# Performance work log

Hardware: AMD Instinct MI355X
Metric: run time of the kernel (lower is better)

Reference implementation:

```python
import jax, jax.numpy as jnp
import numpy as np

B, S = 2, 1024
V, H = 32000, 1024
NH, NKV = 16, 8
HD = H // NH          # 64
L = 8
I = 4 * H             # 4096
EPS = 1e-6
THETA = 10000.0
NEG = -1e9


def setup_inputs() -> dict:
    key = jax.random.key(0)
    ks = jax.random.split(key, 12)
    std = 0.02
    f = lambda k, shape: jax.random.normal(k, shape, jnp.float32) * std
    return {
        "input_ids": jax.random.randint(ks[0], (B, S), 0, V, dtype=jnp.int32),
        "embed": f(ks[1], (V, H)),
        "Wq": f(ks[2], (L, H, NH * HD)),
        "Wk": f(ks[3], (L, H, NKV * HD)),
        "Wv": f(ks[4], (L, H, NKV * HD)),
        "Wo": f(ks[5], (L, NH * HD, H)),
        "Wg": f(ks[6], (L, H, I)),
        "Wu": f(ks[7], (L, H, I)),
        "Wd": f(ks[8], (L, I, H)),
        "ln1": jnp.ones((L, H), jnp.float32),
        "ln2": jnp.ones((L, H), jnp.float32),
        "norm_w": jnp.ones((H,), jnp.float32),
        "lm_head": f(ks[9], (H, V)),
    }


def _rmsnorm(x, w):
    var = jnp.mean(x * x, axis=-1, keepdims=True)
    return x * jax.lax.rsqrt(var + EPS) * w


def _rotate_half(x):
    x1, x2 = jnp.split(x, 2, axis=-1)
    return jnp.concatenate((-x2, x1), axis=-1)


def reference(input_ids, embed, Wq, Wk, Wv, Wo, Wg, Wu, Wd, ln1, ln2, norm_w, lm_head):
    # RoPE tables [S, HD] (freqs duplicated, matching cat((freqs, freqs)))
    inv_freq = 1.0 / (THETA ** (jnp.arange(0, HD, 2, dtype=jnp.float32) / HD))
    t = jnp.arange(S, dtype=jnp.float32)
    freqs = t[:, None] * inv_freq[None, :]
    emb = jnp.concatenate((freqs, freqs), axis=-1)
    cos = jnp.cos(emb)[None, None]  # [1,1,S,HD]
    sin = jnp.sin(emb)[None, None]
    # causal mask [S, S]
    mask = jnp.where(jnp.tril(jnp.ones((S, S), bool)), 0.0, NEG).astype(jnp.float32)

    def layer(h, p):
        wq, wk, wv, wo, wg, wu, wd, g1, g2 = p
        x = _rmsnorm(h, g1)
        q = (x @ wq).reshape(B, S, NH, HD).transpose(0, 2, 1, 3)   # [B,NH,S,HD]
        k = (x @ wk).reshape(B, S, NKV, HD).transpose(0, 2, 1, 3)  # [B,NKV,S,HD]
        v = (x @ wv).reshape(B, S, NKV, HD).transpose(0, 2, 1, 3)
        q = q * cos + _rotate_half(q) * sin
        k = k * cos + _rotate_half(k) * sin
        rep = NH // NKV
        k = jnp.repeat(k, rep, axis=1)  # GQA repeat_interleave
        v = jnp.repeat(v, rep, axis=1)
        scores = jnp.einsum("bhqd,bhkd->bhqk", q, k) / np.sqrt(HD) + mask
        probs = jax.nn.softmax(scores, axis=-1)
        o = jnp.einsum("bhqk,bhkd->bhqd", probs, v)
        o = o.transpose(0, 2, 1, 3).reshape(B, S, NH * HD)
        h = h + o @ wo
        x = _rmsnorm(h, g2)
        h = h + (jax.nn.silu(x @ wg) * (x @ wu)) @ wd
        return h, None

    h = embed[input_ids]  # [B,S,H]
    h, _ = jax.lax.scan(layer, h, (Wq, Wk, Wv, Wo, Wg, Wu, Wd, ln1, ln2))
    h = _rmsnorm(h, norm_w)
    return h @ lm_head  # logits [B,S,V]
```

## Files before the change

### kernel.cpp

```cpp
#include <hip/hip_runtime.h>


typedef unsigned short u16;
typedef __bf16  bf16x8 __attribute__((ext_vector_type(8)));
typedef unsigned short u16x8 __attribute__((ext_vector_type(8)));
typedef float   f32x4  __attribute__((ext_vector_type(4)));

#define DEV static __device__ __forceinline__

constexpr int NB  = 2;
constexpr int S   = 1024;
constexpr int NT  = NB * S;
constexpr int H   = 1024;
constexpr int NH  = 16;
constexpr int NKV = 8;
constexpr int HD  = 64;
constexpr int NL  = 8;
constexpr int FF  = 4096;
constexpr int V   = 32000;
constexpr int QKVW = 2048;

DEV float b2f(u16 x) { return __uint_as_float(((unsigned)x) << 16); }
DEV u16   f2b(float f) {
  unsigned i = __float_as_uint(f);
  return (u16)((i + 0x7fffu + ((i >> 16) & 1u)) >> 16);
}

DEV void gload16(const void* g, void* l) {
  __builtin_amdgcn_global_load_lds(
      (const __attribute__((address_space(1))) void*)g,
      (__attribute__((address_space(3))) void*)l, 16, 0, 0);
}

DEV bf16x8 ld128(const u16* p) { return *reinterpret_cast<const bf16x8*>(p); }

template <int EPI>
__global__ __launch_bounds__(512, 2) void gemm256_k(
    const u16* __restrict__ A, int lda,
    const u16* __restrict__ Bt, int ldb,
    void* __restrict__ C, int ldc, int K)
{
  __shared__ __align__(16) u16 Asm[4][256 * 32];
  __shared__ __align__(16) u16 Bsm[4][256 * 32];

  const int tid  = threadIdx.x;
  const int lane = tid & 63;
  const int lrow = lane & 15;
  const int g    = lane >> 4;
  const int wid  = tid >> 6;
  const int wm   = wid >> 2, wn = wid & 3;

  int flat = blockIdx.y * gridDim.x + blockIdx.x;
  const int cpx = (gridDim.x * gridDim.y) >> 3;
  flat = (flat & 7) * cpx + (flat >> 3);
  const int bx = flat % gridDim.x;
  const int by = flat / gridDim.x;

  const int r0   = tid >> 2, pp = tid & 3;
  const int row1 = 128 + (tid >> 2);
  const int p0 = pp ^ ((r0 ^ (r0 >> 2)) & 3);
  const int p1 = pp ^ ((row1 ^ (row1 >> 2)) & 3);
  const u16* aS0 = A  + (size_t)(bx * 256 + r0)   * lda + p0 * 8;
  const u16* aS1 = A  + (size_t)(bx * 256 + row1) * lda + p1 * 8;
  const u16* bS0 = Bt + (size_t)(by * 256 + r0)   * ldb + p0 * 8;
  const u16* bS1 = Bt + (size_t)(by * 256 + row1) * ldb + p1 * 8;
  const int aB0 = tid * 16, aB1 = (512 + tid) * 16;

  int aOff[8], bOff[4];
  #pragma unroll
  for (int fm = 0; fm < 8; fm++) {
    const int r = wm * 128 + fm * 16 + lrow;
    aOff[fm] = r * 32 + (g ^ ((r ^ (r >> 2)) & 3)) * 8;
  }
  #pragma unroll
  for (int fn = 0; fn < 4; fn++) {
    const int r = wn * 64 + fn * 16 + lrow;
    bOff[fn] = r * 32 + (g ^ ((r ^ (r >> 2)) & 3)) * 8;
  }

  f32x4 acc[8][4] = {};
  const int ntk = K / 32;

  #pragma unroll
  for (int ts = 0; ts < 3; ts++) {
    const long kt = (long)ts * 32;
    gload16(aS0 + kt, (char*)Asm[ts] + aB0);
    gload16(bS0 + kt, (char*)Bsm[ts] + aB0);
    gload16(aS1 + kt, (char*)Asm[ts] + aB1);
    gload16(bS1 + kt, (char*)Bsm[ts] + aB1);
  }
  asm volatile("s_waitcnt vmcnt(8)" ::: "memory");
  __builtin_amdgcn_s_barrier();

#define KTILE(VMW, STG)                                                         \
  {                                                                             \
    const int rs = t & 3, ss = (t + 3) & 3;                                     \
    const long kt = (long)(t + 3) * 32;                                         \
    bf16x8 af[4], bf[4];                                                        \
    _Pragma("unroll") for (int i = 0; i < 4; i++) bf[i] = ld128(&Bsm[rs][bOff[i]]); \
    _Pragma("unroll") for (int i = 0; i < 4; i++) af[i] = ld128(&Asm[rs][aOff[i]]); \
    if (STG) { gload16(aS0 + kt, (char*)Asm[ss] + aB0);                         \
               gload16(bS0 + kt, (char*)Bsm[ss] + aB0); }                       \
    __builtin_amdgcn_s_barrier();                                               \
    asm volatile("s_waitcnt lgkmcnt(0)" ::: "memory");                          \
    __builtin_amdgcn_sched_barrier(0);                                          \
    __builtin_amdgcn_s_setprio(1);                                              \
    _Pragma("unroll") for (int m = 0; m < 4; m++)                               \
      _Pragma("unroll") for (int n = 0; n < 4; n++)                             \
        acc[m][n] = __builtin_amdgcn_mfma_f32_16x16x32_bf16(af[m], bf[n], acc[m][n], 0, 0, 0); \
    __builtin_amdgcn_s_setprio(0);                                              \
    __builtin_amdgcn_s_barrier();                                               \
    _Pragma("unroll") for (int i = 0; i < 4; i++) af[i] = ld128(&Asm[rs][aOff[4 + i]]); \
    if (STG) { gload16(aS1 + kt, (char*)Asm[ss] + aB1);                         \
               gload16(bS1 + kt, (char*)Bsm[ss] + aB1); }                       \
    __builtin_amdgcn_s_barrier();                                               \
    asm volatile("s_waitcnt lgkmcnt(0)" ::: "memory");                          \
    __builtin_amdgcn_sched_barrier(0);                                          \
    __builtin_amdgcn_s_setprio(1);                                              \
    _Pragma("unroll") for (int m = 0; m < 4; m++)                               \
      _Pragma("unroll") for (int n = 0; n < 4; n++)                             \
        acc[4 + m][n] = __builtin_amdgcn_mfma_f32_16x16x32_bf16(af[m], bf[n], acc[4 + m][n], 0, 0, 0); \
    __builtin_amdgcn_s_setprio(0);                                              \
    VMW;                                                                        \
    __builtin_amdgcn_sched_barrier(0);                                          \
    __builtin_amdgcn_s_barrier();                                               \
  }

  {
    int t = 0;
    for (; t < ntk - 3; ++t) KTILE(asm volatile("s_waitcnt vmcnt(8)" ::: "memory"), true);
    KTILE(asm volatile("s_waitcnt vmcnt(4)" ::: "memory"), false); ++t;
    KTILE(asm volatile("s_waitcnt vmcnt(0)" ::: "memory"), false); ++t;
    KTILE((void)0, false);
  }
#undef KTILE

  if (EPI == 2) {
    #pragma unroll
    for (int fm = 0; fm < 8; fm++) {
      #pragma unroll
      for (int fp = 0; fp < 2; fp++) {
        #pragma unroll
        for (int r = 0; r < 4; r++) {
          const size_t row = bx * 256 + wm * 128 + fm * 16 + g * 4 + r;
          const int nb = by * 256 + wn * 64 + fp * 32;
          const int oc = (nb >> 5) * 16 + lrow;
          const float gg = acc[fm][2 * fp][r];
          const float uu = acc[fm][2 * fp + 1][r];
          ((u16*)C)[row * ldc + oc] = f2b(gg / (1.f + __expf(-gg)) * uu);
        }
      }
    }
  } else {
    #pragma unroll
    for (int fm = 0; fm < 8; fm++) {
      #pragma unroll
      for (int fn = 0; fn < 4; fn++) {
        #pragma unroll
        for (int r = 0; r < 4; r++) {
          const size_t row = bx * 256 + wm * 128 + fm * 16 + g * 4 + r;
          const size_t col = by * 256 + wn * 64 + fn * 16 + lrow;
          ((float*)C)[row * ldc + col] = acc[fm][fn][r];
        }
      }
    }
  }
}

template <int BM, int BN, int WM, int WN, int EPI>
__global__ __launch_bounds__(256) void gemm_k(
    const u16* __restrict__ A, int lda,
    const u16* __restrict__ Bt, int ldb,
    void* __restrict__ C, int ldc,
    const float2* __restrict__ tab, int K)
{
  __shared__ __align__(16) u16 As[BM * 32];
  __shared__ __align__(16) u16 Bs[BN * 32];

  const int tid  = threadIdx.x;
  const int lane = tid & 63;
  const int lrow = lane & 15;
  const int kb   = lane >> 4;
  const int w    = tid >> 6;
  const int wm   = w / WN, wn = w % WN;
  constexpr int WR = BM / WM, WC = BN / WN;
  constexpr int FM = WR / 16, FN = WC / 16;

  const u16* Ap = A + blockIdx.x * BM * lda;
  const u16* Bp = Bt + blockIdx.y * BN * ldb;

  f32x4 acc[FM][FN] = {};

  for (int k0 = 0; k0 < K; k0 += 32) {
    #pragma unroll
    for (int i = 0; i < (BM * 4) / 256; i++) {
      const int c = i * 256 + tid;
      gload16(Ap + (c >> 2) * lda + k0 + (c & 3) * 8, (char*)As + c * 16);
    }
    #pragma unroll
    for (int i = 0; i < (BN * 4) / 256; i++) {
      const int c = i * 256 + tid;
      gload16(Bp + (c >> 2) * ldb + k0 + (c & 3) * 8, (char*)Bs + c * 16);
    }
    __syncthreads();

    bf16x8 af[FM], bfv[FN];
    #pragma unroll
    for (int fm = 0; fm < FM; fm++)
      af[fm] = *reinterpret_cast<const bf16x8*>(As + (wm * WR + fm * 16 + lrow) * 32 + kb * 8);
    #pragma unroll
    for (int fn = 0; fn < FN; fn++)
      bfv[fn] = *reinterpret_cast<const bf16x8*>(Bs + (wn * WC + fn * 16 + lrow) * 32 + kb * 8);

    #pragma unroll
    for (int fm = 0; fm < FM; fm++) {
      #pragma unroll
      for (int fn = 0; fn < FN; fn++) {
        acc[fm][fn] = __builtin_amdgcn_mfma_f32_16x16x32_bf16(af[fm], bfv[fn], acc[fm][fn], 0, 0, 0);
      }
    }
    __syncthreads();
  }

  if (EPI == 4) {
    const int colb = blockIdx.y * BN + wn * WC;
    const int head = colb >> 6;
    const float qs = (head < 16) ? 0.125f : 1.0f;
    #pragma unroll
    for (int fm = 0; fm < FM; fm++) {
      #pragma unroll
      for (int r = 0; r < 4; r++) {
        const int row = blockIdx.x * BM + wm * WR + fm * 16 + kb * 4 + r;
        if (head >= 24) {
          #pragma unroll
          for (int fn = 0; fn < FN; fn++)
            ((u16*)C)[row * ldc + colb + fn * 16 + lrow] = f2b(acc[fm][fn][r]);
        } else {
          const int s = row & (S - 1);
          #pragma unroll
          for (int fp = 0; fp < 2; fp++) {
            const int d = fp * 16 + lrow;
            const float2 cs = tab[s * 32 + d];
            const float x1 = acc[fm][fp][r];
            const float x2 = acc[fm][fp + 2][r];
            ((u16*)C)[row * ldc + colb + d]      = f2b((x1 * cs.x - x2 * cs.y) * qs);
            ((u16*)C)[row * ldc + colb + d + 32] = f2b((x2 * cs.x + x1 * cs.y) * qs);
          }
        }
      }
    }
  } else {
    #pragma unroll
    for (int fm = 0; fm < FM; fm++) {
      #pragma unroll
      for (int fn = 0; fn < FN; fn++) {
        #pragma unroll
        for (int r = 0; r < 4; r++) {
          const int row = blockIdx.x * BM + wm * WR + fm * 16 + kb * 4 + r;
          const int col = blockIdx.y * BN + wn * WC + fn * 16 + lrow;
          ((u16*)C)[row * ldc + col] = f2b(acc[fm][fn][r]);
        }
      }
    }
  }
}

__global__ __launch_bounds__(256) void transpose_k(
    const float* __restrict__ W, u16* __restrict__ WT, int K, int N, int rmode,
    size_t wstride, size_t tstride)
{
  __shared__ float t[32][33];
  const float* Wp = W + (size_t)blockIdx.z * wstride;
  u16* WTp = WT + (size_t)blockIdx.z * tstride;
  const int k0 = blockIdx.x * 32, n0 = blockIdx.y * 32;
  const int tx = threadIdx.x & 31, ty = threadIdx.x >> 5;
  #pragma unroll
  for (int i = 0; i < 32; i += 8)
    t[ty + i][tx] = Wp[(size_t)(k0 + ty + i) * N + (n0 + tx)];
  __syncthreads();
  #pragma unroll
  for (int i = 0; i < 32; i += 8) {
    const int n = n0 + ty + i;
    const int orow = (rmode == 0) ? n : ((n >> 4) * 32 + (n & 15) + ((rmode == 2) ? 16 : 0));
    WTp[(size_t)orow * K + (k0 + tx)] = f2b(t[tx][ty + i]);
  }
}

__global__ __launch_bounds__(256) void embed_k(
    const int* __restrict__ ids, const float* __restrict__ E, float* __restrict__ h)
{
  const int t = blockIdx.x;
  const int id = ids[t];
  ((float4*)(h + t * H))[threadIdx.x] = ((const float4*)(E + (size_t)id * H))[threadIdx.x];
}

__global__ __launch_bounds__(256) void rmsnorm_k(
    const float* __restrict__ h, const float* __restrict__ w, u16* __restrict__ x)
{
  const int row = blockIdx.x;
  const float4 hv = ((const float4*)(h + row * H))[threadIdx.x];
  float s = hv.x * hv.x + hv.y * hv.y + hv.z * hv.z + hv.w * hv.w;
  #pragma unroll
  for (int off = 32; off; off >>= 1) s += __shfl_xor(s, off, 64);
  __shared__ float red[4];
  if ((threadIdx.x & 63) == 0) red[threadIdx.x >> 6] = s;
  __syncthreads();
  s = red[0] + red[1] + red[2] + red[3];
  const float scale = rsqrtf(s * (1.f / H) + 1e-6f);
  const float4 wv = ((const float4*)w)[threadIdx.x];
  ushort4 ov;
  ov.x = f2b(hv.x * scale * wv.x);
  ov.y = f2b(hv.y * scale * wv.y);
  ov.z = f2b(hv.z * scale * wv.z);
  ov.w = f2b(hv.w * scale * wv.w);
  ((ushort4*)(x + row * H))[threadIdx.x] = ov;
}

__global__ __launch_bounds__(256) void addnorm_k(
    float* __restrict__ h, const u16* __restrict__ dl,
    const float* __restrict__ w, u16* __restrict__ x)
{
  const int row = blockIdx.x;
  float4 hv = ((const float4*)(h + row * H))[threadIdx.x];
  const ushort4 dv = ((const ushort4*)(dl + row * H))[threadIdx.x];
  hv.x += b2f(dv.x); hv.y += b2f(dv.y); hv.z += b2f(dv.z); hv.w += b2f(dv.w);
  ((float4*)(h + row * H))[threadIdx.x] = hv;
  float s = hv.x * hv.x + hv.y * hv.y + hv.z * hv.z + hv.w * hv.w;
  #pragma unroll
  for (int off = 32; off; off >>= 1) s += __shfl_xor(s, off, 64);
  __shared__ float red[4];
  if ((threadIdx.x & 63) == 0) red[threadIdx.x >> 6] = s;
  __syncthreads();
  s = red[0] + red[1] + red[2] + red[3];
  const float scale = rsqrtf(s * (1.f / H) + 1e-6f);
  const float4 wv = ((const float4*)w)[threadIdx.x];
  ushort4 ov;
  ov.x = f2b(hv.x * scale * wv.x);
  ov.y = f2b(hv.y * scale * wv.y);
  ov.z = f2b(hv.z * scale * wv.z);
  ov.w = f2b(hv.w * scale * wv.w);
  ((ushort4*)(x + row * H))[threadIdx.x] = ov;
}

__global__ __launch_bounds__(256) void ropetab_k(float2* __restrict__ tab)
{
  const int idx = blockIdx.x * 256 + threadIdx.x;
  const int s = idx >> 5, d = idx & 31;
  const float ang = s * powf(10000.f, -(2.f * d) / 64.f);
  float sn, cs;
  sincosf(ang, &sn, &cs);
  tab[idx] = make_float2(cs, sn);
}

__global__ __launch_bounds__(256) void fattn_k(
    const u16* __restrict__ qkv, u16* __restrict__ o)
{
  __shared__ __align__(16) u16 Ks[64 * 64];
  __shared__ __align__(16) u16 Vt[64 * 72];
  __shared__ __align__(16) u16 Pw[4][16 * 64];

  const int tid  = threadIdx.x;
  const int lane = tid & 63;
  const int lrow = lane & 15;
  const int g    = lane >> 4;
  const int w    = tid >> 6;
  const int bp = blockIdx.x, by = blockIdx.y;
  const int b = by >> 4, hh = by & 15, kh = hh >> 1;

  for (int half = 0; half < 2; half++) {
    const int bx = half ? (15 - bp) : bp;
    const int q0 = bx * 64;

    bf16x8 aq[2];
    {
      const int qrow = q0 + w * 16 + lrow;
      const u16* qp = qkv + (size_t)(b * S + qrow) * QKVW + hh * 64 + g * 8;
      aq[0] = *reinterpret_cast<const bf16x8*>(qp);
      aq[1] = *reinterpret_cast<const bf16x8*>(qp + 32);
    }

    f32x4 oacc[4] = {};
    float mrow[4], lsum[4];
    #pragma unroll
    for (int r = 0; r < 4; r++) { mrow[r] = -1e30f; lsum[r] = 0.f; }

    const int nt = bx + 1;
    for (int t = 0; t < nt; t++) {
      const int kv0 = t * 64;
      __syncthreads();

      #pragma unroll
      for (int i = 0; i < 2; i++) {
        const int c = i * 256 + tid;
        const int r = c >> 3, p = c & 7;
        gload16(qkv + (size_t)(b * S + kv0 + r) * QKVW + 1024 + kh * 64 + ((p ^ (r & 7)) * 8),
                (char*)Ks + c * 16);
      }
      u16x8 vreg[2];
      #pragma unroll
      for (int i = 0; i < 2; i++) {
        const int c = i * 256 + tid;
        const int k = c >> 3, dch = c & 7;
        vreg[i] = *reinterpret_cast<const u16x8*>(
            qkv + (size_t)(b * S + kv0 + k) * QKVW + 1536 + kh * 64 + dch * 8);
      }
      #pragma unroll
      for (int i = 0; i < 2; i++) {
        const int c = i * 256 + tid;
        const int k = c >> 3, d0 = (c & 7) * 8;
        #pragma unroll
        for (int j = 0; j < 8; j++) {
          const int d = d0 + j;
          Vt[d * 72 + (((k >> 3) ^ (d >> 3)) * 8) + (k & 7)] = vreg[i][j];
        }
      }
      __syncthreads();

      f32x4 sacc[4] = {};
      #pragma unroll
      for (int n = 0; n < 4; n++) {
        const int row = n * 16 + lrow;
        #pragma unroll
        for (int k2 = 0; k2 < 2; k2++) {
          const bf16x8 bk = *reinterpret_cast<const bf16x8*>(
              Ks + row * 64 + (((k2 * 4 + g) ^ (row & 7)) * 8));
          sacc[n] = __builtin_amdgcn_mfma_f32_16x16x32_bf16(aq[k2], bk, sacc[n], 0, 0, 0);
        }
      }

      #pragma unroll
      for (int r = 0; r < 4; r++) {
        const int qglob = q0 + w * 16 + g * 4 + r;
        float sv[4];
        float rm = -1e30f;
        #pragma unroll
        for (int n = 0; n < 4; n++) {
          const int kg = kv0 + n * 16 + lrow;
          sv[n] = (kg <= qglob) ? sacc[n][r] : -1e30f;
          rm = fmaxf(rm, sv[n]);
        }
        #pragma unroll
        for (int mk = 1; mk < 16; mk <<= 1) rm = fmaxf(rm, __shfl_xor(rm, mk, 64));
        const float mnew  = fmaxf(mrow[r], rm);
        const float scale = __expf(mrow[r] - mnew);
        float rs = 0.f;
        u16 pb[4];
        #pragma unroll
        for (int n = 0; n < 4; n++) {
          const float p = __expf(sv[n] - mnew);
          rs += p;
          pb[n] = f2b(p);
        }
        #pragma unroll
        for (int mk = 1; mk < 16; mk <<= 1) rs += __shfl_xor(rs, mk, 64);
        lsum[r] = lsum[r] * scale + rs;
        mrow[r] = mnew;
        #pragma unroll
        for (int dt = 0; dt < 4; dt++) oacc[dt][r] *= scale;
        const int ql = g * 4 + r;
        #pragma unroll
        for (int n = 0; n < 4; n++) {
          const int k = n * 16 + lrow;
          Pw[w][ql * 64 + (((k >> 3) ^ (ql & 7)) * 8) + (k & 7)] = pb[n];
        }
      }

      #pragma unroll
      for (int k2 = 0; k2 < 2; k2++) {
        const bf16x8 pa = *reinterpret_cast<const bf16x8*>(
            &Pw[w][lrow * 64 + (((k2 * 4 + g) ^ (lrow & 7)) * 8)]);
        #pragma unroll
        for (int dt = 0; dt < 4; dt++) {
          const int d = dt * 16 + lrow;
          const bf16x8 vb = *reinterpret_cast<const bf16x8*>(
              &Vt[d * 72 + (((k2 * 4 + g) ^ (d >> 3)) * 8)]);
          oacc[dt] = __builtin_amdgcn_mfma_f32_16x16x32_bf16(pa, vb, oacc[dt], 0, 0, 0);
        }
      }
    }

    #pragma unroll
    for (int dt = 0; dt < 4; dt++) {
      #pragma unroll
      for (int r = 0; r < 4; r++) {
        const int qrow = q0 + w * 16 + g * 4 + r;
        o[(size_t)(b * S + qrow) * H + hh * 64 + dt * 16 + lrow] =
            f2b(oacc[dt][r] / lsum[r]);
      }
    }
  }
}

extern "C" void kernel_launch(void* const* d_in, const int* in_sizes, int n_in,
                              void* d_out, int out_size, void* d_ws, size_t ws_size,
                              hipStream_t stream)
{
  const int*   ids  = (const int*)d_in[0];
  const float* EW   = (const float*)d_in[1];
  const float* Wq   = (const float*)d_in[2];
  const float* Wk   = (const float*)d_in[3];
  const float* Wv   = (const float*)d_in[4];
  const float* Wo   = (const float*)d_in[5];
  const float* Wg   = (const float*)d_in[6];
  const float* Wu   = (const float*)d_in[7];
  const float* Wd   = (const float*)d_in[8];
  const float* ln1  = (const float*)d_in[9];
  const float* ln2  = (const float*)d_in[10];
  const float* nw   = (const float*)d_in[11];
  const float* lmw  = (const float*)d_in[12];
  float* out = (float*)d_out;

  const size_t MB = 1u << 20;
  char* ws = (char*)d_ws;
  float*  h   = (float*)(ws);
  u16*    x   = (u16*)(ws + 8 * MB);
  u16*    qkv = (u16*)(ws + 12 * MB);
  u16*    o   = (u16*)(ws + 20 * MB);
  u16*    dl  = (u16*)(ws + 24 * MB);
  u16*    ub  = (u16*)(ws + 28 * MB);
  float2* tab = (float2*)(ws + 44 * MB);
  char*   wb  = ws + 45 * MB;

  const size_t sqkv = (size_t)QKVW * H;
  const size_t swo  = (size_t)H * H;
  const size_t sgu  = (size_t)2 * FF * H;
  const size_t swd  = (size_t)H * FF;

  const bool full = ws_size >= 349 * MB;
  if (!full && ws_size < 108 * MB) return;

  u16 *wqkvT, *woT, *wguT, *wdT, *lmT;
  if (full) {
    wqkvT = (u16*)wb;
    woT   = wqkvT + NL * sqkv;
    wguT  = woT + NL * swo;
    wdT   = wguT + NL * sgu;
    lmT   = wdT + NL * swd;
  } else {
    wqkvT = (u16*)wb;
    woT   = wqkvT + sqkv;
    wguT  = woT + swo;
    wdT   = wguT + sgu;
    lmT   = (u16*)wb;
  }

  auto xpose = [&](int l0, int lz, bool dense) {
    const size_t tq = dense ? sqkv : 0, to = dense ? swo : 0;
    const size_t tg = dense ? sgu : 0,  td = dense ? swd : 0;
    transpose_k<<<dim3(H / 32, H / 32, lz), 256, 0, stream>>>(
        Wq + (size_t)l0 * H * H, wqkvT + (size_t)l0 * tq, H, H, 0, (size_t)H * H, tq);
    transpose_k<<<dim3(H / 32, 512 / 32, lz), 256, 0, stream>>>(
        Wk + (size_t)l0 * H * 512, wqkvT + (size_t)l0 * tq + (size_t)1024 * H, H, 512, 0,
        (size_t)H * 512, tq);
    transpose_k<<<dim3(H / 32, 512 / 32, lz), 256, 0, stream>>>(
        Wv + (size_t)l0 * H * 512, wqkvT + (size_t)l0 * tq + (size_t)1536 * H, H, 512, 0,
        (size_t)H * 512, tq);
    transpose_k<<<dim3(H / 32, H / 32, lz), 256, 0, stream>>>(
        Wo + (size_t)l0 * H * H, woT + (size_t)l0 * to, H, H, 0, (size_t)H * H, to);
    transpose_k<<<dim3(H / 32, FF / 32, lz), 256, 0, stream>>>(
        Wg + (size_t)l0 * H * FF, wguT + (size_t)l0 * tg, H, FF, 1, (size_t)H * FF, tg);
    transpose_k<<<dim3(H / 32, FF / 32, lz), 256, 0, stream>>>(
        Wu + (size_t)l0 * H * FF, wguT + (size_t)l0 * tg, H, FF, 2, (size_t)H * FF, tg);
    transpose_k<<<dim3(FF / 32, H / 32, lz), 256, 0, stream>>>(
        Wd + (size_t)l0 * FF * H, wdT + (size_t)l0 * td, FF, H, 0, (size_t)FF * H, td);
  };

  embed_k<<<NT, 256, 0, stream>>>(ids, EW, h);
  ropetab_k<<<(S * 32) / 256, 256, 0, stream>>>(tab);

  if (full) {
    xpose(0, NL, true);
    transpose_k<<<dim3(H / 32, V / 32, 1), 256, 0, stream>>>(lmw, lmT, H, V, 0, 0, 0);
  }

  rmsnorm_k<<<NT, 256, 0, stream>>>(h, ln1, x);

  for (int l = 0; l < NL; l++) {
    if (!full) xpose(l, 1, false);
    u16* pq = wqkvT + (full ? (size_t)l * sqkv : 0);
    u16* po = woT   + (full ? (size_t)l * swo  : 0);
    u16* pg = wguT  + (full ? (size_t)l * sgu  : 0);
    u16* pd = wdT   + (full ? (size_t)l * swd  : 0);

    gemm_k<64, 128, 2, 2, 4><<<dim3(NT / 64, QKVW / 128), 256, 0, stream>>>(
        x, H, pq, H, qkv, QKVW, tab, H);
    fattn_k<<<dim3(8, NB * NH), 256, 0, stream>>>(qkv, o);
    gemm_k<64, 64, 2, 2, 0><<<dim3(NT / 64, H / 64), 256, 0, stream>>>(
        o, H, po, H, dl, H, nullptr, H);
    addnorm_k<<<NT, 256, 0, stream>>>(h, dl, ln2 + l * H, x);

    gemm256_k<2><<<dim3(NT / 256, (2 * FF) / 256), 512, 0, stream>>>(
        x, H, pg, H, ub, FF, H);
    gemm_k<64, 64, 2, 2, 0><<<dim3(NT / 64, H / 64), 256, 0, stream>>>(
        ub, FF, pd, FF, dl, H, nullptr, FF);
    const float* nxt = (l + 1 < NL) ? (ln1 + (l + 1) * H) : nw;
    addnorm_k<<<NT, 256, 0, stream>>>(h, dl, nxt, x);
  }

  if (!full)
    transpose_k<<<dim3(H / 32, V / 32, 1), 256, 0, stream>>>(lmw, lmT, H, V, 0, 0, 0);
  gemm256_k<3><<<dim3(NT / 256, V / 256), 512, 0, stream>>>(
      x, H, lmT, H, out, V, H);
}
```

Baseline: 2.010 ms.

## Launch one block per query tile with longest-first ordering and lazy softmax rescale

The attention kernel stops pairing two query tiles per block and instead launches 512 blocks, one per (batch, head, query tile). Blocks are ordered so the longest causal tiles run first and head indices are interleaved across neighbouring block IDs. The online softmax now rescales the accumulator and running sum only when some row's new maximum exceeds the stored one by more than 8, which removes exp and multiply work on most tiles. The lazy rescale lets probabilities reach up to e^8 before renormalisation, which carries an overflow or precision risk in bf16 P values. Giving up the paired-tile scheme may also reduce per-block load balance.

```diff
diff --git a/kernel.cpp b/kernel.cpp
--- a/kernel.cpp
+++ b/kernel.cpp
@@ -364,129 +364,144 @@
   const int lrow = lane & 15;
   const int g    = lane >> 4;
   const int w    = tid >> 6;
-  const int bp = blockIdx.x, by = blockIdx.y;
-  const int b = by >> 4, hh = by & 15, kh = hh >> 1;
-
-  for (int half = 0; half < 2; half++) {
-    const int bx = half ? (15 - bp) : bp;
-    const int q0 = bx * 64;
-
-    bf16x8 aq[2];
-    {
-      const int qrow = q0 + w * 16 + lrow;
-      const u16* qp = qkv + (size_t)(b * S + qrow) * QKVW + hh * 64 + g * 8;
-      aq[0] = *reinterpret_cast<const bf16x8*>(qp);
-      aq[1] = *reinterpret_cast<const bf16x8*>(qp + 32);
-    }
-
-    f32x4 oacc[4] = {};
-    float mrow[4], lsum[4];
-    #pragma unroll
-    for (int r = 0; r < 4; r++) { mrow[r] = -1e30f; lsum[r] = 0.f; }
-
-    const int nt = bx + 1;
-    for (int t = 0; t < nt; t++) {
-      const int kv0 = t * 64;
-      __syncthreads();
-
-      #pragma unroll
-      for (int i = 0; i < 2; i++) {
-        const int c = i * 256 + tid;
-        const int r = c >> 3, p = c & 7;
-        gload16(qkv + (size_t)(b * S + kv0 + r) * QKVW + 1024 + kh * 64 + ((p ^ (r & 7)) * 8),
-                (char*)Ks + c * 16);
-      }
-      u16x8 vreg[2];
-      #pragma unroll
-      for (int i = 0; i < 2; i++) {
-        const int c = i * 256 + tid;
-        const int k = c >> 3, dch = c & 7;
-        vreg[i] = *reinterpret_cast<const u16x8*>(
-            qkv + (size_t)(b * S + kv0 + k) * QKVW + 1536 + kh * 64 + dch * 8);
-      }
-      #pragma unroll
-      for (int i = 0; i < 2; i++) {
-        const int c = i * 256 + tid;
-        const int k = c >> 3, d0 = (c & 7) * 8;
-        #pragma unroll
-        for (int j = 0; j < 8; j++) {
-          const int d = d0 + j;
-          Vt[d * 72 + (((k >> 3) ^ (d >> 3)) * 8) + (k & 7)] = vreg[i][j];
-        }
-      }
-      __syncthreads();
-
-      f32x4 sacc[4] = {};
+
+  const int bid = blockIdx.x;
+  const int j   = bid >> 3;
+  const int bh  = (bid & 7) * 4 + (j & 3);
+  const int bx  = 15 - (j >> 2);
+  const int b = bh >> 4, hh = bh & 15, kh = hh >> 1;
+  const int q0 = bx * 64;
+
+  bf16x8 aq[2];
+  {
+    const int qrow = q0 + w * 16 + lrow;
+    const u16* qp = qkv + (size_t)(b * S + qrow) * QKVW + hh * 64 + g * 8;
+    aq[0] = *reinterpret_cast<const bf16x8*>(qp);
+    aq[1] = *reinterpret_cast<const bf16x8*>(qp + 32);
+  }
+
+  f32x4 oacc[4] = {};
+  float mrow[4], lsum[4];
+  #pragma unroll
+  for (int r = 0; r < 4; r++) { mrow[r] = -1e30f; lsum[r] = 0.f; }
+
+  const int nt = bx + 1;
+  for (int t = 0; t < nt; t++) {
+    const int kv0 = t * 64;
+    __syncthreads();
+
+    #pragma unroll
+    for (int i = 0; i < 2; i++) {
+      const int c = i * 256 + tid;
+      const int r = c >> 3, p = c & 7;
+      gload16(qkv + (size_t)(b * S + kv0 + r) * QKVW + 1024 + kh * 64 + ((p ^ (r & 7)) * 8),
+              (char*)Ks + c * 16);
+    }
+    u16x8 vreg[2];
+    #pragma unroll
+    for (int i = 0; i < 2; i++) {
+      const int c = i * 256 + tid;
+      const int k = c >> 3, dch = c & 7;
+      vreg[i] = *reinterpret_cast<const u16x8*>(
+          qkv + (size_t)(b * S + kv0 + k) * QKVW + 1536 + kh * 64 + dch * 8);
+    }
+    #pragma unroll
+    for (int i = 0; i < 2; i++) {
+      const int c = i * 256 + tid;
+      const int k = c >> 3, d0 = (c & 7) * 8;
+      #pragma unroll
+      for (int j2 = 0; j2 < 8; j2++) {
+        const int d = d0 + j2;
+        Vt[d * 72 + (((k >> 3) ^ (d >> 3)) * 8) + (k & 7)] = vreg[i][j2];
+      }
+    }
+    __syncthreads();
+
+    f32x4 sacc[4] = {};
+    #pragma unroll
+    for (int n = 0; n < 4; n++) {
+      const int row = n * 16 + lrow;
+      #pragma unroll
+      for (int k2 = 0; k2 < 2; k2++) {
+        const bf16x8 bk = *reinterpret_cast<const bf16x8*>(
+            Ks + row * 64 + (((k2 * 4 + g) ^ (row & 7)) * 8));
+        sacc[n] = __builtin_amdgcn_mfma_f32_16x16x32_bf16(aq[k2], bk, sacc[n], 0, 0, 0);
+      }
+    }
+
+    float rmv[4];
+    #pragma unroll
+    for (int r = 0; r < 4; r++) {
+      const int qglob = q0 + w * 16 + g * 4 + r;
+      float rm = -1e30f;
       #pragma unroll
       for (int n = 0; n < 4; n++) {
-        const int row = n * 16 + lrow;
-        #pragma unroll
-        for (int k2 = 0; k2 < 2; k2++) {
-          const bf16x8 bk = *reinterpret_cast<const bf16x8*>(
-              Ks + row * 64 + (((k2 * 4 + g) ^ (row & 7)) * 8));
-          sacc[n] = __builtin_amdgcn_mfma_f32_16x16x32_bf16(aq[k2], bk, sacc[n], 0, 0, 0);
-        }
-      }
-
+        const int kg = kv0 + n * 16 + lrow;
+        if (kg > qglob) sacc[n][r] = -1e30f;
+        rm = fmaxf(rm, sacc[n][r]);
+      }
+      #pragma unroll
+      for (int mk = 1; mk < 16; mk <<= 1) rm = fmaxf(rm, __shfl_xor(rm, mk, 64));
+      rmv[r] = rm;
+    }
+
+    int need = 0;
+    #pragma unroll
+    for (int r = 0; r < 4; r++) need |= (rmv[r] > mrow[r] + 8.f) ? 1 : 0;
+    if (__any(need)) {
       #pragma unroll
       for (int r = 0; r < 4; r++) {
-        const int qglob = q0 + w * 16 + g * 4 + r;
-        float sv[4];
-        float rm = -1e30f;
-        #pragma unroll
-        for (int n = 0; n < 4; n++) {
-          const int kg = kv0 + n * 16 + lrow;
-          sv[n] = (kg <= qglob) ? sacc[n][r] : -1e30f;
-          rm = fmaxf(rm, sv[n]);
-        }
-        #pragma unroll
-        for (int mk = 1; mk < 16; mk <<= 1) rm = fmaxf(rm, __shfl_xor(rm, mk, 64));
-        const float mnew  = fmaxf(mrow[r], rm);
+        const float mnew  = fmaxf(mrow[r], rmv[r]);
         const float scale = __expf(mrow[r] - mnew);
-        float rs = 0.f;
-        u16 pb[4];
-        #pragma unroll
-        for (int n = 0; n < 4; n++) {
-          const float p = __expf(sv[n] - mnew);
-          rs += p;
-          pb[n] = f2b(p);
-        }
-        #pragma unroll
-        for (int mk = 1; mk < 16; mk <<= 1) rs += __shfl_xor(rs, mk, 64);
-        lsum[r] = lsum[r] * scale + rs;
         mrow[r] = mnew;
+        lsum[r] *= scale;
         #pragma unroll
         for (int dt = 0; dt < 4; dt++) oacc[dt][r] *= scale;
-        const int ql = g * 4 + r;
-        #pragma unroll
-        for (int n = 0; n < 4; n++) {
-          const int k = n * 16 + lrow;
-          Pw[w][ql * 64 + (((k >> 3) ^ (ql & 7)) * 8) + (k & 7)] = pb[n];
-        }
-      }
-
-      #pragma unroll
-      for (int k2 = 0; k2 < 2; k2++) {
-        const bf16x8 pa = *reinterpret_cast<const bf16x8*>(
-            &Pw[w][lrow * 64 + (((k2 * 4 + g) ^ (lrow & 7)) * 8)]);
-        #pragma unroll
-        for (int dt = 0; dt < 4; dt++) {
-          const int d = dt * 16 + lrow;
-          const bf16x8 vb = *reinterpret_cast<const bf16x8*>(
-              &Vt[d * 72 + (((k2 * 4 + g) ^ (d >> 3)) * 8)]);
-          oacc[dt] = __builtin_amdgcn_mfma_f32_16x16x32_bf16(pa, vb, oacc[dt], 0, 0, 0);
-        }
-      }
-    }
-
-    #pragma unroll
-    for (int dt = 0; dt < 4; dt++) {
-      #pragma unroll
-      for (int r = 0; r < 4; r++) {
-        const int qrow = q0 + w * 16 + g * 4 + r;
-        o[(size_t)(b * S + qrow) * H + hh * 64 + dt * 16 + lrow] =
-            f2b(oacc[dt][r] / lsum[r]);
-      }
+      }
+    }
+
+    #pragma unroll
+    for (int r = 0; r < 4; r++) {
+      float rs = 0.f;
+      u16 pb[4];
+      #pragma unroll
+      for (int n = 0; n < 4; n++) {
+        const float p = __expf(sacc[n][r] - mrow[r]);
+        rs += p;
+        pb[n] = f2b(p);
+      }
+      #pragma unroll
+      for (int mk = 1; mk < 16; mk <<= 1) rs += __shfl_xor(rs, mk, 64);
+      lsum[r] += rs;
+      const int ql = g * 4 + r;
+      #pragma unroll
+      for (int n = 0; n < 4; n++) {
+        const int k = n * 16 + lrow;
+        Pw[w][ql * 64 + (((k >> 3) ^ (ql & 7)) * 8) + (k & 7)] = pb[n];
+      }
+    }
+
+    #pragma unroll
+    for (int k2 = 0; k2 < 2; k2++) {
+      const bf16x8 pa = *reinterpret_cast<const bf16x8*>(
+          &Pw[w][lrow * 64 + (((k2 * 4 + g) ^ (lrow & 7)) * 8)]);
+      #pragma unroll
+      for (int dt = 0; dt < 4; dt++) {
+        const int d = dt * 16 + lrow;
+        const bf16x8 vb = *reinterpret_cast<const bf16x8*>(
+            &Vt[d * 72 + (((k2 * 4 + g) ^ (d >> 3)) * 8)]);
+        oacc[dt] = __builtin_amdgcn_mfma_f32_16x16x32_bf16(pa, vb, oacc[dt], 0, 0, 0);
+      }
+    }
+  }
+
+  #pragma unroll
+  for (int dt = 0; dt < 4; dt++) {
+    #pragma unroll
+    for (int r = 0; r < 4; r++) {
+      const int qrow = q0 + w * 16 + g * 4 + r;
+      o[(size_t)(b * S + qrow) * H + hh * 64 + dt * 16 + lrow] =
+          f2b(oacc[dt][r] / lsum[r]);
     }
   }
 }
@@ -584,7 +599,7 @@
 
     gemm_k<64, 128, 2, 2, 4><<<dim3(NT / 64, QKVW / 128), 256, 0, stream>>>(
         x, H, pq, H, qkv, QKVW, tab, H);
-    fattn_k<<<dim3(8, NB * NH), 256, 0, stream>>>(qkv, o);
+    fattn_k<<<dim3(512), 256, 0, stream>>>(qkv, o);
     gemm_k<64, 64, 2, 2, 0><<<dim3(NT / 64, H / 64), 256, 0, stream>>>(
         o, H, po, H, dl, H, nullptr, H);
     addnorm_k<<<NT, 256, 0, stream>>>(h, dl, ln2 + l * H, x);
```

Result: no change. 1.987 ms (-1.1%).
